# Kernel tuning notes

Hardware: AMD Instinct MI355X
Metric: run time of the kernel (lower is better)

## Reference

```python
import jax, jax.numpy as jnp
import numpy as np

S = 8    # number of path-segments
U = 32   # per-segment input width (subscript 'u')
V = 32   # per-segment output width (subscript 'v')
C = 32   # number of weight groups (indexed dimension)
Z = 65536  # number of rows


def setup_inputs() -> dict:
    key = jax.random.key(0)
    k1, k2, k3 = jax.random.split(key, 3)
    input1 = jax.random.normal(k1, (C, S * U * V), dtype=jnp.float32) * 0.05  # grouped weights
    input2 = jax.random.normal(k2, (Z, S * U), dtype=jnp.float32)             # row features
    counts = jnp.full((C,), Z // C, dtype=jnp.int32)                          # rows per group, contiguous
    coefficients = jax.random.uniform(k3, (S,), dtype=jnp.float32, minval=0.5, maxval=1.5)
    return {"input1": input1, "input2": input2, "counts": counts, "coefficients": coefficients}


def reference(input1, input2, counts, coefficients):
    # Segment-indexed grouped linear: rows are contiguous per group (sizes = counts).
    # For each path-segment s: out_s[z, v] = coeff_s * sum_u x_s[z, u] * W_s[g(z), u, v]
    # Final output concatenates the S segment outputs along the last dim.
    seg_ids = jnp.repeat(jnp.arange(C, dtype=jnp.int32), counts, total_repeat_length=Z)  # [Z]
    outs = []
    for s in range(S):
        W = input1[:, s * U * V:(s + 1) * U * V].reshape(C, U, V)  # [C,U,V]
        x = input2[:, s * U:(s + 1) * U]                           # [Z,U]
        Wz = W[seg_ids]                                            # [Z,U,V] gather by group
        outs.append(coefficients[s] * jnp.einsum('zu,zuv->zv', x, Wz))
    return jnp.concatenate(outs, axis=-1)  # [Z, S*V]
```

## Files before the change

kernel.cpp:

```cpp
#include <hip/hip_runtime.h>


constexpr int S = 8, U = 32, V = 32, C = 32, Z = 65536;
constexpr int BZ = 128;
constexpr int NT = 128;
constexpr int ZS = BZ + 4;
constexpr int WS = 36;

typedef float f4 __attribute__((ext_vector_type(4)));

__global__ __launch_bounds__(NT) void IndexedLinear_kernel(
    const float* __restrict__ W_all,
    const float* __restrict__ X,
    const int*   __restrict__ counts,
    const float* __restrict__ coeff,
    float*       __restrict__ out)
{
  const int tid = threadIdx.x;
  const int s   = blockIdx.x & 7;
  const int zb  = blockIdx.x >> 3;
  const int z0  = zb * BZ;

  __shared__ float XT[U * ZS];
  __shared__ float Wl[U * WS];
  __shared__ int   pre[C + 1];
  __shared__ int   sseg0, suni;

  if (tid <= C) {
    int a = 0;
    for (int i = 0; i < tid; ++i) a += counts[i];
    pre[tid] = a;
  }
  __syncthreads();

  if (tid == 0) {
    int a = 0, b = 0;
    #pragma unroll
    for (int i = 1; i < C; ++i) {
      if (pre[i] <= z0) a = i;
      if (pre[i] <= z0 + BZ - 1) b = i;
    }
    sseg0 = a;
    suni  = (a == b);
  }
  __syncthreads();

  const int   seg0 = sseg0;
  const int   uni  = suni;
  const float cs   = coeff[s];

  const int ug = tid & 7;
  const int zl = tid >> 3;
  f4 xv[8];
  const float* xbase = X + (size_t)z0 * (S * U) + s * U + ug * 4;
  #pragma unroll
  for (int p = 0; p < 8; ++p) {
    xv[p] = *(const f4*)(xbase + (size_t)(p * 16 + zl) * (S * U));
  }

  {
    const float* wbase = W_all + (size_t)seg0 * (S * U * V) + s * (U * V);
    #pragma unroll
    for (int k = 0; k < 2; ++k) {
      const int idx = tid + k * NT;
      f4 wv = *(const f4*)(wbase + idx * 4);
      wv *= cs;
      const int wu = idx >> 3, wc = (idx & 7) * 4;
      *(f4*)&Wl[wu * WS + wc] = wv;
    }
  }

  #pragma unroll
  for (int p = 0; p < 8; ++p) {
    const int z = p * 16 + zl;
    #pragma unroll
    for (int j = 0; j < 4; ++j) XT[(ug * 4 + j) * ZS + z] = xv[p][j];
  }
  __syncthreads();

  const int vg = tid & 7;
  const int zg = tid >> 3;
  float acc[8][4] = {};

  if (uni) {
    #pragma unroll
    for (int u = 0; u < U; ++u) {
      const f4 w  = *(const f4*)&Wl[u * WS + vg * 4];
      const f4 xa = *(const f4*)&XT[u * ZS + zg * 8];
      const f4 xb = *(const f4*)&XT[u * ZS + zg * 8 + 4];
      #pragma unroll
      for (int j = 0; j < 4; ++j) {
        #pragma unroll
        for (int i = 0; i < 4; ++i) {
          acc[i][j]     += xa[i] * w[j];
          acc[4 + i][j] += xb[i] * w[j];
        }
      }
    }
  } else {
    #pragma unroll 1
    for (int zi = 0; zi < 8; ++zi) {
      const int z = z0 + zg * 8 + zi;
      int sg = 0;
      #pragma unroll 1
      for (int i = 1; i < C; ++i) if (pre[i] <= z) sg = i;
      const float* wb = W_all + (size_t)sg * (S * U * V) + s * (U * V) + vg * 4;
      #pragma unroll 1
      for (int u = 0; u < U; ++u) {
        const float xs = XT[u * ZS + zg * 8 + zi];
        #pragma unroll
        for (int j = 0; j < 4; ++j) acc[zi][j] += xs * wb[u * V + j];
      }
      #pragma unroll
      for (int j = 0; j < 4; ++j) acc[zi][j] *= cs;
    }
  }

  float* ob = out + (size_t)(z0 + zg * 8) * (S * V) + s * V + vg * 4;
  #pragma unroll
  for (int zi = 0; zi < 8; ++zi) {
    f4 o;
    o[0] = acc[zi][0]; o[1] = acc[zi][1]; o[2] = acc[zi][2]; o[3] = acc[zi][3];
    *(f4*)(ob + (size_t)zi * (S * V)) = o;
  }
}

extern "C" void kernel_launch(void* const* d_in, const int* in_sizes, int n_in,
                              void* d_out, int out_size, void* d_ws, size_t ws_size,
                              hipStream_t stream) {
  const float* input1       = (const float*)d_in[0];
  const float* input2       = (const float*)d_in[1];
  const int*   counts       = (const int*)d_in[2];
  const float* coefficients = (const float*)d_in[3];
  float*       out          = (float*)d_out;

  const int grid = (Z / BZ) * S;
  IndexedLinear_kernel<<<grid, NT, 0, stream>>>(input1, input2, counts,
                                                coefficients, out);
}
```

Measured before the change: 128.6 us.

## Rewrite grouped linear as per-wave 32x32 bf16 MFMA tiles

Replaces the LDS-tiled FP32 outer-product kernel with one wavefront per 32-row by segment tile. Each tile uses two bf16 32x32x16 MFMA instructions, with X and coefficient-scaled W converted to bf16 in registers. Group lookup now uses a wave-level shuffle prefix scan and ballot instead of shared memory and barriers, and loads and stores are nontemporal. This removes LDS staging and syncs and moves the math onto matrix cores. In exchange it lowers precision to bf16 inputs and reloads W per wave with strided scalar loads.

```diff
diff --git a/kernel.cpp b/kernel.cpp
--- a/kernel.cpp
+++ b/kernel.cpp
@@ -2,12 +2,19 @@
 
 
 constexpr int S = 8, U = 32, V = 32, C = 32, Z = 65536;
-constexpr int BZ = 128;
-constexpr int NT = 128;
-constexpr int ZS = BZ + 4;
-constexpr int WS = 36;
+constexpr int SU = S * U;
+constexpr int SV = S * V;
+constexpr int NT = 256;
 
-typedef float f4 __attribute__((ext_vector_type(4)));
+typedef float  f4    __attribute__((ext_vector_type(4)));
+typedef float  f32x16 __attribute__((ext_vector_type(16)));
+typedef short  bf16x8 __attribute__((ext_vector_type(8)));
+
+__device__ __forceinline__ short f2bf(float f) {
+  unsigned u = __builtin_bit_cast(unsigned, f);
+  u = (u + 0x7FFFu + ((u >> 16) & 1u)) >> 16;
+  return (short)u;
+}
 
 __global__ __launch_bounds__(NT) void IndexedLinear_kernel(
     const float* __restrict__ W_all,
@@ -16,112 +23,85 @@
     const float* __restrict__ coeff,
     float*       __restrict__ out)
 {
-  const int tid = threadIdx.x;
-  const int s   = blockIdx.x & 7;
-  const int zb  = blockIdx.x >> 3;
-  const int z0  = zb * BZ;
+  const int lane = threadIdx.x & 63;
+  const int g    = blockIdx.x * (NT / 64) + (threadIdx.x >> 6);
+  const int s    = g & 7;
+  const int z0   = (g >> 3) * 32;
 
-  __shared__ float XT[U * ZS];
-  __shared__ float Wl[U * WS];
-  __shared__ int   pre[C + 1];
-  __shared__ int   sseg0, suni;
+  const int m = lane & 31;
+  const int h = lane >> 5;
 
-  if (tid <= C) {
-    int a = 0;
-    for (int i = 0; i < tid; ++i) a += counts[i];
-    pre[tid] = a;
+  const float* xr = X + (size_t)(z0 + m) * SU + s * U;
+  f4 xa = __builtin_nontemporal_load((const f4*)(xr + 8 * h));
+  f4 xb = __builtin_nontemporal_load((const f4*)(xr + 8 * h + 4));
+  f4 xc = __builtin_nontemporal_load((const f4*)(xr + 16 + 8 * h));
+  f4 xd = __builtin_nontemporal_load((const f4*)(xr + 16 + 8 * h + 4));
+
+  int c = (lane < C) ? counts[lane] : 0;
+  int inc = c;
+  #pragma unroll
+  for (int d = 1; d < 32; d <<= 1) {
+    int o = __shfl_up(inc, d, 64);
+    if (lane >= d) inc += o;
   }
-  __syncthreads();
+  const int exc = inc - c;
+  const unsigned long long ma = __ballot(lane < C && exc <= z0);
+  const unsigned long long mb = __ballot(lane < C && exc <= z0 + 31);
+  const int segA = __popcll(ma) - 1;
+  const int segB = __popcll(mb) - 1;
 
-  if (tid == 0) {
-    int a = 0, b = 0;
+  const float cs = coeff[s];
+
+  if (segA == segB) {
+    const float* wb = W_all + (size_t)segA * (S * U * V) + s * (U * V);
+
+    bf16x8 b1, b2;
     #pragma unroll
-    for (int i = 1; i < C; ++i) {
-      if (pre[i] <= z0) a = i;
-      if (pre[i] <= z0 + BZ - 1) b = i;
+    for (int j = 0; j < 8; ++j)
+      b1[j] = f2bf(wb[(8 * h + j) * V + m] * cs);
+    #pragma unroll
+    for (int j = 0; j < 8; ++j)
+      b2[j] = f2bf(wb[(16 + 8 * h + j) * V + m] * cs);
+
+    bf16x8 a1, a2;
+    #pragma unroll
+    for (int i = 0; i < 4; ++i) {
+      a1[i]     = f2bf(xa[i]);
+      a1[4 + i] = f2bf(xb[i]);
+      a2[i]     = f2bf(xc[i]);
+      a2[4 + i] = f2bf(xd[i]);
     }
-    sseg0 = a;
-    suni  = (a == b);
-  }
-  __syncthreads();
 
-  const int   seg0 = sseg0;
-  const int   uni  = suni;
-  const float cs   = coeff[s];
+    f32x16 acc = {};
+    acc = __builtin_amdgcn_mfma_f32_32x32x16_bf16(a1, b1, acc, 0, 0, 0);
+    acc = __builtin_amdgcn_mfma_f32_32x32x16_bf16(a2, b2, acc, 0, 0, 0);
 
-  const int ug = tid & 7;
-  const int zl = tid >> 3;
-  f4 xv[8];
-  const float* xbase = X + (size_t)z0 * (S * U) + s * U + ug * 4;
-  #pragma unroll
-  for (int p = 0; p < 8; ++p) {
-    xv[p] = *(const f4*)(xbase + (size_t)(p * 16 + zl) * (S * U));
-  }
-
-  {
-    const float* wbase = W_all + (size_t)seg0 * (S * U * V) + s * (U * V);
+    float* ob = out + (size_t)z0 * SV + s * V + m;
     #pragma unroll
-    for (int k = 0; k < 2; ++k) {
-      const int idx = tid + k * NT;
-      f4 wv = *(const f4*)(wbase + idx * 4);
-      wv *= cs;
-      const int wu = idx >> 3, wc = (idx & 7) * 4;
-      *(f4*)&Wl[wu * WS + wc] = wv;
-    }
-  }
-
-  #pragma unroll
-  for (int p = 0; p < 8; ++p) {
-    const int z = p * 16 + zl;
-    #pragma unroll
-    for (int j = 0; j < 4; ++j) XT[(ug * 4 + j) * ZS + z] = xv[p][j];
-  }
-  __syncthreads();
-
-  const int vg = tid & 7;
-  const int zg = tid >> 3;
-  float acc[8][4] = {};
-
-  if (uni) {
-    #pragma unroll
-    for (int u = 0; u < U; ++u) {
-      const f4 w  = *(const f4*)&Wl[u * WS + vg * 4];
-      const f4 xa = *(const f4*)&XT[u * ZS + zg * 8];
-      const f4 xb = *(const f4*)&XT[u * ZS + zg * 8 + 4];
-      #pragma unroll
-      for (int j = 0; j < 4; ++j) {
-        #pragma unroll
-        for (int i = 0; i < 4; ++i) {
-          acc[i][j]     += xa[i] * w[j];
-          acc[4 + i][j] += xb[i] * w[j];
-        }
-      }
+    for (int r = 0; r < 16; ++r) {
+      const int row = (r & 3) + 8 * (r >> 2) + 4 * h;
+      __builtin_nontemporal_store(acc[r], ob + (size_t)row * SV);
     }
   } else {
+    const int zz = z0 + m;
+    int sg = 0;
     #pragma unroll 1
-    for (int zi = 0; zi < 8; ++zi) {
-      const int z = z0 + zg * 8 + zi;
-      int sg = 0;
-      #pragma unroll 1
-      for (int i = 1; i < C; ++i) if (pre[i] <= z) sg = i;
-      const float* wb = W_all + (size_t)sg * (S * U * V) + s * (U * V) + vg * 4;
-      #pragma unroll 1
-      for (int u = 0; u < U; ++u) {
-        const float xs = XT[u * ZS + zg * 8 + zi];
-        #pragma unroll
-        for (int j = 0; j < 4; ++j) acc[zi][j] += xs * wb[u * V + j];
-      }
+    for (int i = 1; i < C; ++i) {
+      const int pi = __shfl(exc, i, 64);
+      if (pi <= zz) sg = i;
+    }
+    const float* wr = W_all + (size_t)sg * (S * U * V) + s * (U * V) + 16 * h;
+    const float* xrow = X + (size_t)zz * SU + s * U;
+    float accv[16] = {};
+    #pragma unroll 1
+    for (int u = 0; u < U; ++u) {
+      const float xu = xrow[u];
       #pragma unroll
-      for (int j = 0; j < 4; ++j) acc[zi][j] *= cs;
+      for (int j = 0; j < 16; ++j) accv[j] += xu * wr[u * V + j];
     }
-  }
-
-  float* ob = out + (size_t)(z0 + zg * 8) * (S * V) + s * V + vg * 4;
-  #pragma unroll
-  for (int zi = 0; zi < 8; ++zi) {
-    f4 o;
-    o[0] = acc[zi][0]; o[1] = acc[zi][1]; o[2] = acc[zi][2]; o[3] = acc[zi][3];
-    *(f4*)(ob + (size_t)zi * (S * V)) = o;
+    float* ob = out + (size_t)zz * SV + s * V + 16 * h;
+    #pragma unroll
+    for (int j = 0; j < 16; ++j) ob[j] = accv[j] * cs;
   }
 }
 
@@ -134,7 +114,8 @@
   const float* coefficients = (const float*)d_in[3];
   float*       out          = (float*)d_out;
 
-  const int grid = (Z / BZ) * S;
+  const int tiles = (Z / 32) * S;
+  const int grid  = tiles / (NT / 64);
   IndexedLinear_kernel<<<grid, NT, 0, stream>>>(input1, input2, counts,
                                                 coefficients, out);
 }
```

Result: slower. 136.3 us (+5.9%).
